# Kernel optimization log

Hardware: AMD Instinct MI355X
Metric: run time of the kernel (lower is better)

The kernel has to match this reference:

```python
import jax, jax.numpy as jnp
import numpy as np

CONV_SPECS = [(1, 64, 4, 2), (64, 128, 8, 4), (128, 256, 10, 5), (256, 256, 12, 6)]  # (cin, cout, k, stride)
N_CODEBOOKS = 8
CODEBOOK_SIZE = 1024
D_MODEL = 256
STATE_FRAMES = 4
B = 8192


def setup_inputs() -> dict:
    key = jax.random.key(0)
    ks = jax.random.split(key, 3 + 2 * len(CONV_SPECS) + 1)
    d = {
        "audio_frame": jax.random.normal(ks[0], (B, 1, 240), dtype=jnp.float32),
        "state_in": jax.random.normal(ks[1], (B, D_MODEL, STATE_FRAMES), dtype=jnp.float32),
    }
    for i, (cin, cout, k, s) in enumerate(CONV_SPECS):
        scale = 1.0 / np.sqrt(cin * k)
        d[f"W{i}"] = jax.random.normal(ks[2 + 2 * i], (cout, cin, k), dtype=jnp.float32) * scale
        d[f"b{i}"] = jnp.zeros((cout,), dtype=jnp.float32)
    d["codebooks"] = jax.random.normal(ks[-1], (N_CODEBOOKS, CODEBOOK_SIZE, D_MODEL), dtype=jnp.float32) * 0.02
    return d


def _causal_conv(x, W, b, stride):
    # x: [B, Cin, L]; causal left-pad of (k - stride) so L_out = L // stride
    k = W.shape[-1]
    x = jnp.pad(x, ((0, 0), (0, 0), (k - stride, 0)))
    y = jax.lax.conv_general_dilated(
        x, W, window_strides=(stride,), padding="VALID",
        dimension_numbers=("NCH", "OIH", "NCH"))
    return y + b[None, :, None]


def _rvq_indices(x_btd, codebooks):
    # x_btd: [B, T, D]; codebooks: [Q, K, D] -> indices [B, Q, T]
    r = x_btd
    idxs = []
    for q in range(codebooks.shape[0]):
        cb = codebooks[q]                                        # [K, D]
        # ||r - c||^2 = ||r||^2 - 2 r.c + ||c||^2 ; ||r||^2 constant over k for argmin
        dist = jnp.sum(cb * cb, axis=-1) - 2.0 * jnp.einsum("btd,kd->btk", r, cb)
        idx = jnp.argmin(dist, axis=-1)                          # [B, T]
        r = r - cb[idx]                                          # residual update
        idxs.append(idx)
    return jnp.stack(idxs, axis=1)                               # [B, Q, T]


def reference(audio_frame, state_in, W0, b0, W1, b1, W2, b2, W3, b3, codebooks):
    # state: roll left, zero last frame
    new_state = jnp.roll(state_in, -1, axis=2).at[:, :, -1].set(0.0)

    # causal conv encoder stack (ELU between conv blocks)
    Ws, bs = (W0, W1, W2, W3), (b0, b1, b2, b3)
    x = audio_frame
    for i, (_, _, _, stride) in enumerate(CONV_SPECS):
        x = _causal_conv(x, Ws[i], bs[i], stride)
        if i < len(CONV_SPECS) - 1:
            x = jax.nn.elu(x)
    # x: [B, D_MODEL, 1]

    new_state = new_state.at[:, :, -1].set(x[:, :, -1])

    z = _rvq_indices(x.transpose(0, 2, 1), codebooks)            # [B, Q, T]
    acoustic_tokens = z[:, :, -1]                                # [B, 8]
    return acoustic_tokens, new_state
```

## Files before the change

### kernel.cpp

```cpp
#include <hip/hip_runtime.h>
#include <hip/hip_bf16.h>

#define GB 4

__device__ __forceinline__ float elu1(float v) { return v > 0.f ? v : expm1f(v); }

__global__ void cnorm_kernel(const float* __restrict__ cb, float* __restrict__ cnorm) {
    int g = blockIdx.x * blockDim.x + threadIdx.x;
    if (g >= 8 * 1024) return;
    const float* p = cb + (size_t)g * 256;
    float s = 0.f;
    for (int d = 0; d < 256; d += 4) {
        float4 v = *reinterpret_cast<const float4*>(p + d);
        s += v.x * v.x + v.y * v.y + v.z * v.z + v.w * v.w;
    }
    cnorm[g] = s;
}

__global__ void cbtrans_kernel(const float* __restrict__ cb, float* __restrict__ cbT) {
    int t = blockIdx.x * blockDim.x + threadIdx.x;
    int o = t * 4;
    const int s = o >> 13;
    const int r = o & 8191;
    const int dl = r >> 10;
    const int k = r & 1023;
    const int q = s >> 5;
    const int d = (s & 31) * 8 + dl;
    const float* src = cb + ((size_t)(q * 1024 + k)) * 256 + d;
    float4 v;
    v.x = src[0 * 256]; v.y = src[1 * 256]; v.z = src[2 * 256]; v.w = src[3 * 256];
    *reinterpret_cast<float4*>(cbT + o) = v;
}

__global__ void wtrans_kernel(const float* __restrict__ W1, const float* __restrict__ W2,
                              const float* __restrict__ W3, float* __restrict__ W1c,
                              float* __restrict__ W2c, float* __restrict__ W3c) {
    int g = blockIdx.x * blockDim.x + threadIdx.x;
    if (g < 16384) {
        int ci = g >> 8, io = (g >> 6) & 3, cg = g & 63;
        int c = cg + (io >> 1) * 64;
        const float* src = W1 + c * 512 + ci * 8 + (io & 1) * 4;
        *reinterpret_cast<float4*>(W1c + g * 4) =
            *reinterpret_cast<const float4*>(src);
    }
    int g2 = g - 16384;
    if (g2 >= 0 && g2 < 98304) {
        int ci = g2 / 768, rem = g2 % 768;
        int jq = rem >> 8, c = rem & 255;
        float v[4];
#pragma unroll
        for (int e = 0; e < 4; ++e) {
            int j = jq * 4 + e;
            v[e] = (j < 10) ? W2[c * 1280 + ci * 10 + j] : 0.f;
        }
        float4 o; o.x = v[0]; o.y = v[1]; o.z = v[2]; o.w = v[3];
        *reinterpret_cast<float4*>(W2c + g2 * 4) = o;
    }
    int g3 = g - 16384 - 98304;
    if (g3 >= 0 && g3 < 196608) {
        int ci = g3 / 768, rem = g3 % 768;
        int jq = rem >> 8, c = rem & 255;
        const float* src = W3 + c * 3072 + ci * 12 + 6 + jq * 2;
        W3c[g3 * 2] = src[0];
        W3c[g3 * 2 + 1] = src[1];
    }
}

__global__ __launch_bounds__(256, 2)
void convA_kernel(const float* __restrict__ audio,
                  const float* __restrict__ W0, const float* __restrict__ b0,
                  const float* __restrict__ W1c, const float* __restrict__ b1,
                  float* __restrict__ y1g) {
    __shared__ __align__(16) float xs[244];
    __shared__ __align__(16) float y0s[2 * 64 * 124];

    const int tid = threadIdx.x;
    const int bbase = blockIdx.x * 2;

    if (tid < 128) {
        const int bz = tid >> 6, ciz = tid & 63;
        float* p = y0s + (bz * 64 + ciz) * 124;
        p[0] = 0.f; p[1] = 0.f; p[2] = 0.f; p[3] = 0.f;
    }

    for (int bi2 = 0; bi2 < 2; ++bi2) {
        __syncthreads();
        if (tid < 242) xs[tid] = (tid < 2) ? 0.f : audio[(bbase + bi2) * 240 + tid - 2];
        __syncthreads();
        const int ci = tid >> 2, tg = tid & 3;
        float4 w = *reinterpret_cast<const float4*>(W0 + ci * 4);
        float bias = b0[ci];
        for (int t = tg; t < 120; t += 4) {
            float v = bias + w.x * xs[2 * t] + w.y * xs[2 * t + 1]
                           + w.z * xs[2 * t + 2] + w.w * xs[2 * t + 3];
            y0s[(bi2 * 64 + ci) * 124 + 4 + t] = elu1(v);
        }
    }
    __syncthreads();
    {
        const int bi = tid >> 7;
        const int half = (tid >> 6) & 1;
        const int cg = tid & 63;
        const int t0 = 15 * half;
        float acc0[15], acc1[15];
        const float bias0 = b1[cg], bias1 = b1[cg + 64];
#pragma unroll
        for (int u = 0; u < 15; ++u) { acc0[u] = bias0; acc1[u] = bias1; }
        const float* w1base = W1c + cg * 4;
        const float* ybase = y0s + bi * 64 * 124 + 4 * t0;
        for (int ci = 0; ci < 64; ++ci) {
            float4 wA0 = *reinterpret_cast<const float4*>(w1base + (ci * 4 + 0) * 256);
            float4 wB0 = *reinterpret_cast<const float4*>(w1base + (ci * 4 + 1) * 256);
            float4 wA1 = *reinterpret_cast<const float4*>(w1base + (ci * 4 + 2) * 256);
            float4 wB1 = *reinterpret_cast<const float4*>(w1base + (ci * 4 + 3) * 256);
            const float* yb = ybase + ci * 124;
            float4 row4[16];
#pragma unroll
            for (int j = 0; j < 16; ++j)
                row4[j] = *reinterpret_cast<const float4*>(yb + 4 * j);
#pragma unroll
            for (int u = 0; u < 15; ++u) {
                acc0[u] += wA0.x * row4[u].x + wA0.y * row4[u].y
                         + wA0.z * row4[u].z + wA0.w * row4[u].w
                         + wB0.x * row4[u + 1].x + wB0.y * row4[u + 1].y
                         + wB0.z * row4[u + 1].z + wB0.w * row4[u + 1].w;
                acc1[u] += wA1.x * row4[u].x + wA1.y * row4[u].y
                         + wA1.z * row4[u].z + wA1.w * row4[u].w
                         + wB1.x * row4[u + 1].x + wB1.y * row4[u + 1].y
                         + wB1.z * row4[u + 1].z + wB1.w * row4[u + 1].w;
            }
        }
        const int b = bbase + bi;
        float* yo0 = y1g + ((size_t)b * 128 + cg) * 32 + t0;
        float* yo1 = y1g + ((size_t)b * 128 + cg + 64) * 32 + t0;
#pragma unroll
        for (int u = 0; u < 15; ++u) {
            yo0[u] = elu1(acc0[u]);
            yo1[u] = elu1(acc1[u]);
        }
    }
}

__global__ __launch_bounds__(256, 2)
void convB_kernel(const float* __restrict__ state_in,
                  const float* __restrict__ b2, const float* __restrict__ b3,
                  const float* __restrict__ W2c, const float* __restrict__ W3c,
                  const float* __restrict__ y1g,
                  float* __restrict__ out, float* __restrict__ r_ws) {
    __shared__ __align__(16) float y2s[GB * 256 * 6];

    const int tid = threadIdx.x;
    const int bbase = blockIdx.x * GB;

    {
        const int c = tid;
        float acc[GB][6];
        float bias = b2[c];
#pragma unroll
        for (int bi = 0; bi < GB; ++bi)
#pragma unroll
            for (int t = 0; t < 6; ++t) acc[bi][t] = bias;
        const float* w2base = W2c + c * 4;
        for (int ci = 0; ci < 128; ++ci) {
            float4 a0 = *reinterpret_cast<const float4*>(w2base + (ci * 3 + 0) * 1024);
            float4 a1 = *reinterpret_cast<const float4*>(w2base + (ci * 3 + 1) * 1024);
            float4 a2 = *reinterpret_cast<const float4*>(w2base + (ci * 3 + 2) * 1024);
            const float w[10] = {a0.x, a0.y, a0.z, a0.w, a1.x,
                                 a1.y, a1.z, a1.w, a2.x, a2.y};
#pragma unroll
            for (int bi = 0; bi < GB; ++bi) {
                const float* yr = y1g + ((size_t)(bbase + bi) * 128 + ci) * 32;
                float row[32];
#pragma unroll
                for (int k4 = 0; k4 < 8; ++k4) {
                    float4 v = *reinterpret_cast<const float4*>(yr + k4 * 4);
                    row[k4 * 4] = v.x; row[k4 * 4 + 1] = v.y;
                    row[k4 * 4 + 2] = v.z; row[k4 * 4 + 3] = v.w;
                }
                acc[bi][0] += w[5] * row[0] + w[6] * row[1] + w[7] * row[2]
                            + w[8] * row[3] + w[9] * row[4];
#pragma unroll
                for (int t = 1; t < 6; ++t) {
                    const int q0 = 5 * t - 5;
                    float s = 0.f;
#pragma unroll
                    for (int j = 0; j < 10; ++j) s += w[j] * row[q0 + j];
                    acc[bi][t] += s;
                }
            }
        }
#pragma unroll
        for (int bi = 0; bi < GB; ++bi)
#pragma unroll
            for (int t = 0; t < 6; ++t)
                y2s[(bi * 256 + c) * 6 + t] = elu1(acc[bi][t]);
    }
    __syncthreads();
    {
        const int c = tid;
        float acc[GB];
        float bias = b3[c];
#pragma unroll
        for (int bi = 0; bi < GB; ++bi) acc[bi] = bias;
        const float* w3base = W3c + c * 2;
        for (int ci = 0; ci < 256; ++ci) {
            float2 w01 = *reinterpret_cast<const float2*>(w3base + (ci * 3 + 0) * 512);
            float2 w23 = *reinterpret_cast<const float2*>(w3base + (ci * 3 + 1) * 512);
            float2 w45 = *reinterpret_cast<const float2*>(w3base + (ci * 3 + 2) * 512);
#pragma unroll
            for (int bi = 0; bi < GB; ++bi) {
                const float* yr = y2s + (bi * 256 + ci) * 6;
                float2 a = *reinterpret_cast<const float2*>(yr);
                float2 d = *reinterpret_cast<const float2*>(yr + 2);
                float2 e = *reinterpret_cast<const float2*>(yr + 4);
                acc[bi] += w01.x * a.x + w01.y * a.y + w23.x * d.x + w23.y * d.y
                         + w45.x * e.x + w45.y * e.y;
            }
        }
#pragma unroll
        for (int bi = 0; bi < GB; ++bi) {
            const int b = bbase + bi;
            float y3 = acc[bi];
            r_ws[b * 256 + c] = y3;
            float4 si = *reinterpret_cast<const float4*>(state_in + b * 1024 + c * 4);
            float4 o; o.x = si.y; o.y = si.z; o.z = si.w; o.w = y3;
            *reinterpret_cast<float4*>(out + 65536 + b * 1024 + c * 4) = o;
        }
    }
}

__device__ __forceinline__ unsigned long long distkey(float d, int k) {
    unsigned u = __float_as_uint(d);
    u = (u & 0x80000000u) ? ~u : (u | 0x80000000u);
    return ((unsigned long long)u << 32) | (unsigned)k;
}

__global__ __launch_bounds__(256)
void rvq_kernel(const float* __restrict__ cb, const float* __restrict__ cbT,
                const float* __restrict__ cnorm, const float* __restrict__ r_ws,
                float* __restrict__ out) {
    __shared__ __align__(16) float rs[16 * 256];
    __shared__ unsigned long long part_sh[2][16];
    __shared__ int idx_sh[16];

    const int tid = threadIdx.x;
    const int lane = tid & 63;
    const int wid = tid >> 6;
    const int bg = wid >> 1;
    const int kg = wid & 1;
    const int b0 = blockIdx.x * 16;
    const int kb = kg * 512 + 4 * lane;

    for (int it = 0; it < 4; ++it) {
        int o = (it * 256 + tid) * 4;
        *reinterpret_cast<float4*>(rs + o) =
            *reinterpret_cast<const float4*>(r_ws + b0 * 256 + o);
    }
    __syncthreads();

    for (int q = 0; q < 8; ++q) {
        float acc[8][8];
#pragma unroll
        for (int i = 0; i < 8; ++i)
#pragma unroll
            for (int j = 0; j < 8; ++j) acc[i][j] = 0.f;

        for (int ds = 0; ds < 32; ++ds) {
            const float* sb = cbT + (size_t)(q * 32 + ds) * 8192;
#pragma unroll
            for (int dp = 0; dp < 2; ++dp) {
                float4 cv0[4], cv1[4];
#pragma unroll
                for (int dd = 0; dd < 4; ++dd) {
                    const int dl = dp * 4 + dd;
                    cv0[dd] = *reinterpret_cast<const float4*>(sb + dl * 1024 + kb);
                    cv1[dd] = *reinterpret_cast<const float4*>(sb + dl * 1024 + kb + 256);
                }
                float rr[8][4];
#pragma unroll
                for (int i = 0; i < 8; ++i) {
                    float4 t = *reinterpret_cast<const float4*>(
                        rs + (bg * 8 + i) * 256 + ds * 8 + dp * 4);
                    rr[i][0] = t.x; rr[i][1] = t.y; rr[i][2] = t.z; rr[i][3] = t.w;
                }
#pragma unroll
                for (int dd = 0; dd < 4; ++dd) {
#pragma unroll
                    for (int i = 0; i < 8; ++i) {
                        const float r = rr[i][dd];
                        acc[i][0] += r * cv0[dd].x; acc[i][1] += r * cv0[dd].y;
                        acc[i][2] += r * cv0[dd].z; acc[i][3] += r * cv0[dd].w;
                        acc[i][4] += r * cv1[dd].x; acc[i][5] += r * cv1[dd].y;
                        acc[i][6] += r * cv1[dd].z; acc[i][7] += r * cv1[dd].w;
                    }
                }
            }
        }
        {
            float4 cn0 = *reinterpret_cast<const float4*>(cnorm + q * 1024 + kb);
            float4 cn1 = *reinterpret_cast<const float4*>(cnorm + q * 1024 + kb + 256);
            float c0e[4] = {cn0.x, cn0.y, cn0.z, cn0.w};
            float c1e[4] = {cn1.x, cn1.y, cn1.z, cn1.w};
#pragma unroll
            for (int i = 0; i < 8; ++i) {
                unsigned long long k = 0xFFFFFFFFFFFFFFFFull;
#pragma unroll
                for (int e = 0; e < 4; ++e) {
                    unsigned long long ka = distkey(c0e[e] - 2.f * acc[i][e], kb + e);
                    unsigned long long kc = distkey(c1e[e] - 2.f * acc[i][4 + e],
                                                    kb + 256 + e);
                    if (ka < k) k = ka;
                    if (kc < k) k = kc;
                }
                for (int off = 32; off >= 1; off >>= 1) {
                    unsigned long long o = __shfl_xor(k, off, 64);
                    if (o < k) k = o;
                }
                if (lane == 0) part_sh[kg][bg * 8 + i] = k;
            }
        }
        __syncthreads();
        if (tid < 16) {
            unsigned long long ka = part_sh[0][tid];
            unsigned long long kc = part_sh[1][tid];
            if (kc < ka) ka = kc;
            const int idx = (int)(ka & 0xFFFFFFFFu);
            idx_sh[tid] = idx;
            out[(b0 + tid) * 8 + q] = (float)idx;
        }
        __syncthreads();
        for (int it = 0; it < 16; ++it) {
            const int idx = idx_sh[it];
            rs[it * 256 + tid] -= cb[((size_t)(q * 1024 + idx)) * 256 + tid];
        }
        __syncthreads();
    }
}

extern "C" void kernel_launch(void* const* d_in, const int* in_sizes, int n_in,
                              void* d_out, int out_size, void* d_ws, size_t ws_size,
                              hipStream_t stream) {
    const float* audio = (const float*)d_in[0];
    const float* state = (const float*)d_in[1];
    const float* W0 = (const float*)d_in[2];
    const float* b0 = (const float*)d_in[3];
    const float* W1 = (const float*)d_in[4];
    const float* b1 = (const float*)d_in[5];
    const float* W2 = (const float*)d_in[6];
    const float* b2 = (const float*)d_in[7];
    const float* W3 = (const float*)d_in[8];
    const float* b3 = (const float*)d_in[9];
    const float* cbk = (const float*)d_in[10];
    float* out = (float*)d_out;

    float* cnorm_ws = (float*)d_ws;
    float* r_ws = cnorm_ws + 8192;
    float* W1c = r_ws + 2097152;
    float* W2c = W1c + 65536;
    float* W3c = W2c + 393216;
    float* y1g = W3c + 393216;
    float* cbT = y1g + 33554432;

    cnorm_kernel<<<32, 256, 0, stream>>>(cbk, cnorm_ws);
    cbtrans_kernel<<<2048, 256, 0, stream>>>(cbk, cbT);
    wtrans_kernel<<<1216, 256, 0, stream>>>(W1, W2, W3, W1c, W2c, W3c);
    convA_kernel<<<4096, 256, 0, stream>>>(audio, W0, b0, W1c, b1, y1g);
    convB_kernel<<<8192 / GB, 256, 0, stream>>>(state, b2, b3, W2c, W3c, y1g,
                                                out, r_ws);
    rvq_kernel<<<512, 256, 0, stream>>>(cbk, cbT, cnorm_ws, r_ws, out);
}
```

Before: 1.774 ms.

## Remap convB threads to four output channels per thread per batch item

convB now gives each 64-lane wavefront a single batch item, and each thread computes four adjacent output channels, where before each thread handled one channel across four batch items. The y1 row is loaded once per thread and reused across four channels instead of being reloaded for each batch item. Weights are now read per channel group rather than shared across batch items. Blocks shrink to 128 threads covering two batch items, and the grid grows to 4096. This shifts the reuse from weights to activations, cutting y1 global traffic but raising weight loads per FLOP, and register pressure may change.

```diff
diff --git a/kernel.cpp b/kernel.cpp
--- a/kernel.cpp
+++ b/kernel.cpp
@@ -1,7 +1,5 @@
 #include <hip/hip_runtime.h>
 #include <hip/hip_bf16.h>
-
-#define GB 4
 
 __device__ __forceinline__ float elu1(float v) { return v > 0.f ? v : expm1f(v); }
 
@@ -141,43 +139,54 @@
     }
 }
 
-__global__ __launch_bounds__(256, 2)
+__global__ __launch_bounds__(128, 2)
 void convB_kernel(const float* __restrict__ state_in,
                   const float* __restrict__ b2, const float* __restrict__ b3,
                   const float* __restrict__ W2c, const float* __restrict__ W3c,
                   const float* __restrict__ y1g,
                   float* __restrict__ out, float* __restrict__ r_ws) {
-    __shared__ __align__(16) float y2s[GB * 256 * 6];
+    __shared__ __align__(16) float y2s[2 * 256 * 6];
 
     const int tid = threadIdx.x;
-    const int bbase = blockIdx.x * GB;
+    const int bi = tid >> 6;
+    const int lane = tid & 63;
+    const int c0 = lane * 4;
+    const int b = blockIdx.x * 2 + bi;
 
     {
-        const int c = tid;
-        float acc[GB][6];
-        float bias = b2[c];
-#pragma unroll
-        for (int bi = 0; bi < GB; ++bi)
-#pragma unroll
-            for (int t = 0; t < 6; ++t) acc[bi][t] = bias;
-        const float* w2base = W2c + c * 4;
+        float acc[4][6];
+        float4 bv = *reinterpret_cast<const float4*>(b2 + c0);
+        const float be[4] = {bv.x, bv.y, bv.z, bv.w};
+#pragma unroll
+        for (int cc = 0; cc < 4; ++cc)
+#pragma unroll
+            for (int t = 0; t < 6; ++t) acc[cc][t] = be[cc];
+        const float* w2base = W2c + c0 * 4;
+        const float* yb = y1g + (size_t)b * 4096;
         for (int ci = 0; ci < 128; ++ci) {
-            float4 a0 = *reinterpret_cast<const float4*>(w2base + (ci * 3 + 0) * 1024);
-            float4 a1 = *reinterpret_cast<const float4*>(w2base + (ci * 3 + 1) * 1024);
-            float4 a2 = *reinterpret_cast<const float4*>(w2base + (ci * 3 + 2) * 1024);
-            const float w[10] = {a0.x, a0.y, a0.z, a0.w, a1.x,
-                                 a1.y, a1.z, a1.w, a2.x, a2.y};
-#pragma unroll
-            for (int bi = 0; bi < GB; ++bi) {
-                const float* yr = y1g + ((size_t)(bbase + bi) * 128 + ci) * 32;
-                float row[32];
-#pragma unroll
-                for (int k4 = 0; k4 < 8; ++k4) {
-                    float4 v = *reinterpret_cast<const float4*>(yr + k4 * 4);
-                    row[k4 * 4] = v.x; row[k4 * 4 + 1] = v.y;
-                    row[k4 * 4 + 2] = v.z; row[k4 * 4 + 3] = v.w;
-                }
-                acc[bi][0] += w[5] * row[0] + w[6] * row[1] + w[7] * row[2]
+            float row[32];
+#pragma unroll
+            for (int k4 = 0; k4 < 8; ++k4) {
+                float4 v = *reinterpret_cast<const float4*>(yb + ci * 32 + k4 * 4);
+                row[k4 * 4] = v.x; row[k4 * 4 + 1] = v.y;
+                row[k4 * 4 + 2] = v.z; row[k4 * 4 + 3] = v.w;
+            }
+            float4 wq0[4], wq1[4], wq2[4];
+#pragma unroll
+            for (int cc = 0; cc < 4; ++cc) {
+                wq0[cc] = *reinterpret_cast<const float4*>(
+                    w2base + (ci * 3 + 0) * 1024 + cc * 4);
+                wq1[cc] = *reinterpret_cast<const float4*>(
+                    w2base + (ci * 3 + 1) * 1024 + cc * 4);
+                wq2[cc] = *reinterpret_cast<const float4*>(
+                    w2base + (ci * 3 + 2) * 1024 + cc * 4);
+            }
+#pragma unroll
+            for (int cc = 0; cc < 4; ++cc) {
+                const float w[10] = {wq0[cc].x, wq0[cc].y, wq0[cc].z, wq0[cc].w,
+                                     wq1[cc].x, wq1[cc].y, wq1[cc].z, wq1[cc].w,
+                                     wq2[cc].x, wq2[cc].y};
+                acc[cc][0] += w[5] * row[0] + w[6] * row[1] + w[7] * row[2]
                             + w[8] * row[3] + w[9] * row[4];
 #pragma unroll
                 for (int t = 1; t < 6; ++t) {
@@ -185,46 +194,48 @@
                     float s = 0.f;
 #pragma unroll
                     for (int j = 0; j < 10; ++j) s += w[j] * row[q0 + j];
-                    acc[bi][t] += s;
-                }
-            }
-        }
-#pragma unroll
-        for (int bi = 0; bi < GB; ++bi)
+                    acc[cc][t] += s;
+                }
+            }
+        }
+#pragma unroll
+        for (int cc = 0; cc < 4; ++cc)
 #pragma unroll
             for (int t = 0; t < 6; ++t)
-                y2s[(bi * 256 + c) * 6 + t] = elu1(acc[bi][t]);
+                y2s[(bi * 256 + c0 + cc) * 6 + t] = elu1(acc[cc][t]);
     }
     __syncthreads();
     {
-        const int c = tid;
-        float acc[GB];
-        float bias = b3[c];
-#pragma unroll
-        for (int bi = 0; bi < GB; ++bi) acc[bi] = bias;
-        const float* w3base = W3c + c * 2;
+        float acc3[4];
+        float4 bv = *reinterpret_cast<const float4*>(b3 + c0);
+        acc3[0] = bv.x; acc3[1] = bv.y; acc3[2] = bv.z; acc3[3] = bv.w;
+        const float* w3base = W3c + c0 * 2;
+        const float* y2b = y2s + bi * 1536;
         for (int ci = 0; ci < 256; ++ci) {
-            float2 w01 = *reinterpret_cast<const float2*>(w3base + (ci * 3 + 0) * 512);
-            float2 w23 = *reinterpret_cast<const float2*>(w3base + (ci * 3 + 1) * 512);
-            float2 w45 = *reinterpret_cast<const float2*>(w3base + (ci * 3 + 2) * 512);
-#pragma unroll
-            for (int bi = 0; bi < GB; ++bi) {
-                const float* yr = y2s + (bi * 256 + ci) * 6;
-                float2 a = *reinterpret_cast<const float2*>(yr);
-                float2 d = *reinterpret_cast<const float2*>(yr + 2);
-                float2 e = *reinterpret_cast<const float2*>(yr + 4);
-                acc[bi] += w01.x * a.x + w01.y * a.y + w23.x * d.x + w23.y * d.y
-                         + w45.x * e.x + w45.y * e.y;
-            }
-        }
-#pragma unroll
-        for (int bi = 0; bi < GB; ++bi) {
-            const int b = bbase + bi;
-            float y3 = acc[bi];
-            r_ws[b * 256 + c] = y3;
-            float4 si = *reinterpret_cast<const float4*>(state_in + b * 1024 + c * 4);
-            float4 o; o.x = si.y; o.y = si.z; o.z = si.w; o.w = y3;
-            *reinterpret_cast<float4*>(out + 65536 + b * 1024 + c * 4) = o;
+            const float* yr = y2b + ci * 6;
+            float2 a = *reinterpret_cast<const float2*>(yr);
+            float2 d = *reinterpret_cast<const float2*>(yr + 2);
+            float2 e = *reinterpret_cast<const float2*>(yr + 4);
+#pragma unroll
+            for (int cc = 0; cc < 4; ++cc) {
+                float2 w01 = *reinterpret_cast<const float2*>(
+                    w3base + (ci * 3 + 0) * 512 + cc * 2);
+                float2 w23 = *reinterpret_cast<const float2*>(
+                    w3base + (ci * 3 + 1) * 512 + cc * 2);
+                float2 w45 = *reinterpret_cast<const float2*>(
+                    w3base + (ci * 3 + 2) * 512 + cc * 2);
+                acc3[cc] += w01.x * a.x + w01.y * a.y + w23.x * d.x + w23.y * d.y
+                          + w45.x * e.x + w45.y * e.y;
+            }
+        }
+        float4 y3; y3.x = acc3[0]; y3.y = acc3[1]; y3.z = acc3[2]; y3.w = acc3[3];
+        *reinterpret_cast<float4*>(r_ws + b * 256 + c0) = y3;
+#pragma unroll
+        for (int cc = 0; cc < 4; ++cc) {
+            float4 si = *reinterpret_cast<const float4*>(
+                state_in + b * 1024 + (c0 + cc) * 4);
+            float4 o; o.x = si.y; o.y = si.z; o.z = si.w; o.w = acc3[cc];
+            *reinterpret_cast<float4*>(out + 65536 + b * 1024 + (c0 + cc) * 4) = o;
         }
     }
 }
@@ -365,7 +376,7 @@
     cbtrans_kernel<<<2048, 256, 0, stream>>>(cbk, cbT);
     wtrans_kernel<<<1216, 256, 0, stream>>>(W1, W2, W3, W1c, W2c, W3c);
     convA_kernel<<<4096, 256, 0, stream>>>(audio, W0, b0, W1c, b1, y1g);
-    convB_kernel<<<8192 / GB, 256, 0, stream>>>(state, b2, b3, W2c, W3c, y1g,
-                                                out, r_ws);
+    convB_kernel<<<4096, 128, 0, stream>>>(state, b2, b3, W2c, W3c, y1g,
+                                           out, r_ws);
     rvq_kernel<<<512, 256, 0, stream>>>(cbk, cbT, cnorm_ws, r_ws, out);
 }
```

New measurement: 2.431 ms. 1.37x slower.
